# Kernel optimization log

Measured on AMD Instinct MI355X. Metric: run time of the kernel, lower is better.

## Reference

```python
import jax, jax.numpy as jnp
import numpy as np

B, P, K, HE, HF = 256, 128, 512, 1024, 512
D = K + HE + 2 * HF  # 2560, MLP input dim
HID = 64


def setup_inputs() -> dict:
    key = jax.random.key(0)
    ks = jax.random.split(key, 6)
    query = jax.random.normal(ks[0], (B, 1, HE), dtype=jnp.float32)
    keys = jax.random.normal(ks[1], (B, P, K), dtype=jnp.float32)
    frameLSTM_h = jax.random.normal(ks[2], (B, 1, 2 * HF), dtype=jnp.float32)
    mask = jax.random.randint(ks[3], (B, P), 0, 2, dtype=jnp.int32)
    mask = mask.at[:, 0].set(1)  # guarantee at least one unmasked player per row
    W1 = jax.random.normal(ks[4], (D, HID), dtype=jnp.float32) / np.float32(np.sqrt(D))
    W2 = jax.random.normal(ks[5], (HID, 1), dtype=jnp.float32) / np.float32(np.sqrt(HID))
    return dict(query=query, keys=keys, frameLSTM_h=frameLSTM_h, mask=mask, W1=W1, W2=W2)


def reference(query, keys, frameLSTM_h, mask, W1, W2):
    # Faithful to: cat([keys, query.repeat, frame.repeat]) @ W1 -> ReLU -> @ W2.
    # The pre-activation is linear, so splitting W1 by row-blocks is exactly the
    # same math without materializing the repeated/concatenated (B,P,D) tensor.
    W1k = W1[:K]            # (K, 64)
    W1q = W1[K:K + HE]      # (HE, 64)
    W1f = W1[K + HE:]       # (2*HF, 64)
    h = jax.nn.relu(
        jnp.einsum('bpk,kh->bph', keys, W1k)
        + jnp.einsum('boe,eh->boh', query, W1q)        # broadcasts over P
        + jnp.einsum('bof,fh->boh', frameLSTM_h, W1f)  # broadcasts over P
    )  # (B, P, 64)
    raw_scores = jnp.einsum('bph,ho->bp', h, W2)  # (B, P)
    raw_scores = jnp.where(mask == 0, -jnp.inf, raw_scores)
    weights = jax.nn.softmax(raw_scores, axis=1)  # (B, P)
    context = jnp.einsum('bp,bpk->bk', weights, keys)[:, None, :]  # (B, 1, K)
    embeddings = jnp.concatenate([context, frameLSTM_h], axis=2)   # (B, 1, K+2*HF)
    return embeddings, weights
```

## Files before the change

kernel.cpp:

```cpp
#include <hip/hip_runtime.h>
#include <hip/hip_bf16.h>
#include <cstdint>
#include <math.h>


typedef __bf16 bf16;
typedef __attribute__((ext_vector_type(8))) __bf16 bf16x8;
typedef __attribute__((ext_vector_type(4))) float f32x4;

#define NB 256
#define NP 128
#define NK 512
#define SMEM_BYTES (65536 + 8192 + 8192 + 512 + 512 + 65536)

__global__ __launch_bounds__(512, 2) void fused_kernel(
    const float* __restrict__ keys, const float* __restrict__ query,
    const float* __restrict__ frame, const int* __restrict__ mask,
    const float* __restrict__ W1, const float* __restrict__ W2,
    float* __restrict__ out)
{
    extern __shared__ char smem[];
    char* sB      = smem;
    float* sq     = (float*)(smem + 65536);
    float* aux    = sq + 2048;
    float* scores = aux + 2048;
    float* wts    = scores + 128;
    char* kb      = smem + 65536 + 8192 + 8192 + 1024;

    const int b = blockIdx.x;
    const int t = threadIdx.x;
    const int w = t >> 6;
    const int lane = t & 63;
    const int m = lane & 15;
    const int q = lane >> 4;
    const int p0 = w * 16;
    const int xorv = (m & 7) << 4;

    {
        const int d = t * 4;
        const float* src = (d < 1024) ? (query + (size_t)b * 1024 + d)
                                      : (frame + (size_t)b * 1024 + (d - 1024));
        *(float4*)&sq[d] = *(const float4*)src;
    }

    {
#pragma unroll
        for (int i = 0; i < 8; i++) {
            const int id = t + 512 * i;
            const int h = id & 63;
            const int kc = id >> 6;
            float v[8];
#pragma unroll
            for (int j = 0; j < 8; j++)
                v[j] = W1[(size_t)(kc * 8 + j) * 64 + h];
            bf16x8 bv;
#pragma unroll
            for (int j = 0; j < 8; j++) bv[j] = (bf16)v[j];
            *(bf16x8*)(sB + ((h * 1024 + kc * 16) ^ ((h & 7) << 4))) = bv;
        }
    }

    const float* kbase = keys + (size_t)b * (NP * NK);
    float4 kvs[4];
#pragma unroll
    for (int s = 0; s < 4; s++) {
        const int rl = s * 4 + (lane >> 4);
        const int cc = (lane & 15) ^ (rl & 7);
        kvs[s] = *(const float4*)(kbase + (size_t)(p0 + rl) * NK + cc * 4);
    }
    __syncthreads();

    {
        const int s = t >> 4;
        const int j = t & 15;
        const float4* w1f4 = (const float4*)W1;
        float4 pa = {0.f, 0.f, 0.f, 0.f};
#pragma unroll
        for (int bt = 0; bt < 8; bt++) {
            float4 vv[8];
#pragma unroll
            for (int i = 0; i < 8; i++)
                vv[i] = w1f4[(size_t)(512 + s * 64 + bt * 8 + i) * 16 + j];
#pragma unroll
            for (int i = 0; i < 8; i++) {
                const float qv = sq[s * 64 + bt * 8 + i];
                pa.x += qv * vv[i].x; pa.y += qv * vv[i].y;
                pa.z += qv * vv[i].z; pa.w += qv * vv[i].w;
            }
        }
        pa.x += __shfl_xor(pa.x, 16); pa.y += __shfl_xor(pa.y, 16);
        pa.z += __shfl_xor(pa.z, 16); pa.w += __shfl_xor(pa.w, 16);
        pa.x += __shfl_xor(pa.x, 32); pa.y += __shfl_xor(pa.y, 32);
        pa.z += __shfl_xor(pa.z, 32); pa.w += __shfl_xor(pa.w, 32);
        if (lane < 16)
            *(float4*)&aux[w * 64 + lane * 4] = pa;
    }
    __syncthreads();

    float pv[4], wv[4];
#pragma unroll
    for (int nt = 0; nt < 4; nt++) {
        const int h = nt * 16 + m;
        float sacc = 0.f;
#pragma unroll
        for (int ww = 0; ww < 8; ww++) sacc += aux[ww * 64 + h];
        pv[nt] = sacc;
        wv[nt] = W2[h];
    }

    char* kbw = kb + w * 8192;
#pragma unroll
    for (int s = 0; s < 4; s++)
        *(float4*)(kbw + s * 1024 + lane * 16) = kvs[s];

    f32x4 acc[4];
#pragma unroll
    for (int nt = 0; nt < 4; nt++) acc[nt] = (f32x4){0.f, 0.f, 0.f, 0.f};

    bf16x8 Bp[2][4];
#pragma unroll
    for (int nt = 0; nt < 4; nt++)
        Bp[0][nt] = *(const bf16x8*)(sB + nt * 16384 + m * 1024 + ((q * 16) ^ xorv));

#pragma unroll
    for (int c = 0; c < 8; c++) {
        if (c < 7) {
#pragma unroll
            for (int s = 0; s < 4; s++) {
                const int rl = s * 4 + (lane >> 4);
                const int cc = (lane & 15) ^ (rl & 7);
                kvs[s] = *(const float4*)(kbase + (size_t)(p0 + rl) * NK
                                          + (c + 1) * 64 + cc * 4);
            }
        }
        const char* kbr = kbw + (c & 1) * 4096;
#pragma unroll
        for (int kk2 = 0; kk2 < 2; kk2++) {
            const int kkg = c * 2 + kk2;
            const int bc = kkg & 1;
            const int a0 = (m * 256 + kk2 * 128 + q * 32) ^ xorv;
            const float4 f0 = *(const float4*)(kbr + a0);
            const float4 f1 = *(const float4*)(kbr + (a0 ^ 16));
            if (kkg < 15) {
#pragma unroll
                for (int nt = 0; nt < 4; nt++)
                    Bp[bc ^ 1][nt] = *(const bf16x8*)(sB + nt * 16384 + m * 1024
                                      + ((((kkg + 1) * 64) | (q * 16)) ^ xorv));
            }
            bf16x8 Af;
            Af[0] = (bf16)f0.x; Af[1] = (bf16)f0.y;
            Af[2] = (bf16)f0.z; Af[3] = (bf16)f0.w;
            Af[4] = (bf16)f1.x; Af[5] = (bf16)f1.y;
            Af[6] = (bf16)f1.z; Af[7] = (bf16)f1.w;
#pragma unroll
            for (int nt = 0; nt < 4; nt++)
                acc[nt] = __builtin_amdgcn_mfma_f32_16x16x32_bf16(Af, Bp[bc][nt], acc[nt], 0, 0, 0);
        }
        if (c < 7) {
            char* kbwn = kbw + ((c + 1) & 1) * 4096;
#pragma unroll
            for (int s = 0; s < 4; s++)
                *(float4*)(kbwn + s * 1024 + lane * 16) = kvs[s];
        }
    }

    float pr[4] = {0.f, 0.f, 0.f, 0.f};
#pragma unroll
    for (int nt = 0; nt < 4; nt++)
#pragma unroll
        for (int r = 0; r < 4; r++)
            pr[r] += fmaxf(acc[nt][r] + pv[nt], 0.f) * wv[nt];

#pragma unroll
    for (int off = 1; off < 16; off <<= 1)
#pragma unroll
        for (int r = 0; r < 4; r++)
            pr[r] += __shfl_xor(pr[r], off);

    if (m == 0) {
#pragma unroll
        for (int r = 0; r < 4; r++) scores[p0 + q * 4 + r] = pr[r];
    }
    __syncthreads();

    const int cq = t & 127;
    const int pg = t >> 7;
    const float4* kp4 = (const float4*)kbase;
    float4 kv0[8];
#pragma unroll
    for (int i = 0; i < 8; i++)
        kv0[i] = kp4[(size_t)(pg * 32 + i) * 128 + cq];

    if (t < 64) {
        const int pa_ = t, pb_ = t + 64;
        float s0 = (mask[b * 128 + pa_] == 0) ? -INFINITY : scores[pa_];
        float s1 = (mask[b * 128 + pb_] == 0) ? -INFINITY : scores[pb_];
        float mx = fmaxf(s0, s1);
#pragma unroll
        for (int off = 32; off; off >>= 1) mx = fmaxf(mx, __shfl_xor(mx, off));
        float e0 = __expf(s0 - mx), e1 = __expf(s1 - mx);
        float sum = e0 + e1;
#pragma unroll
        for (int off = 32; off; off >>= 1) sum += __shfl_xor(sum, off);
        const float inv = 1.0f / sum;
        e0 *= inv; e1 *= inv;
        wts[pa_] = e0; wts[pb_] = e1;
        float* wout = out + (size_t)NB * 1536;
        wout[b * 128 + pa_] = e0;
        wout[b * 128 + pb_] = e1;
    }
    __syncthreads();

    {
        float4 ca = {0.f, 0.f, 0.f, 0.f};
#pragma unroll
        for (int i = 0; i < 8; i++) {
            const float wvv = wts[pg * 32 + i];
            ca.x += wvv * kv0[i].x; ca.y += wvv * kv0[i].y;
            ca.z += wvv * kv0[i].z; ca.w += wvv * kv0[i].w;
        }
#pragma unroll
        for (int bt = 1; bt < 4; bt++) {
            float4 kv[8];
#pragma unroll
            for (int i = 0; i < 8; i++)
                kv[i] = kp4[(size_t)(pg * 32 + bt * 8 + i) * 128 + cq];
#pragma unroll
            for (int i = 0; i < 8; i++) {
                const float wvv = wts[pg * 32 + bt * 8 + i];
                ca.x += wvv * kv[i].x; ca.y += wvv * kv[i].y;
                ca.z += wvv * kv[i].z; ca.w += wvv * kv[i].w;
            }
        }
        *(float4*)&aux[pg * 512 + cq * 4] = ca;
    }
    __syncthreads();
    if (t < 512)
        out[(size_t)b * 1536 + t] =
            aux[t] + aux[512 + t] + aux[1024 + t] + aux[1536 + t];

    if (t < 256) {
        const float4 fv = *(const float4*)(frame + (size_t)b * 1024 + t * 4);
        *(float4*)(out + (size_t)b * 1536 + 512 + t * 4) = fv;
    }
}

extern "C" void kernel_launch(void* const* d_in, const int* in_sizes, int n_in,
                              void* d_out, int out_size, void* d_ws, size_t ws_size,
                              hipStream_t stream) {
    const float* query = (const float*)d_in[0];
    const float* keys  = (const float*)d_in[1];
    const float* frame = (const float*)d_in[2];
    const int*   mask  = (const int*)d_in[3];
    const float* W1    = (const float*)d_in[4];
    const float* W2    = (const float*)d_in[5];
    float* out = (float*)d_out;

    hipFuncSetAttribute((const void*)fused_kernel,
                        hipFuncAttributeMaxDynamicSharedMemorySize, SMEM_BYTES);

    fused_kernel<<<256, 512, SMEM_BYTES, stream>>>(keys, query, frame, mask,
                                                   W1, W2, out);
}
```

Measured before the change: 123.4 us.

## Stage keys via direct global-to-LDS loads and overlap query projection with MFMA loop

Keys chunks now go straight from global memory into double-buffered LDS through global_load_lds, instead of being loaded into registers and then written to LDS. The query/frame projection against W1, which used to run as a separate phase behind an extra barrier, is now spread across the eight MFMA chunk iterations so its global W1 reads overlap the matrix work. The register double-buffering of the W1 B fragments is dropped, and those fragments are read from LDS right before each MFMA. This lowers register pressure and removes a barrier, at the risk of exposing LDS read latency and depending on correct wait handling for the asynchronous LDS loads.

```diff
diff --git a/kernel.cpp b/kernel.cpp
--- a/kernel.cpp
+++ b/kernel.cpp
@@ -11,7 +11,21 @@
 #define NB 256
 #define NP 128
 #define NK 512
-#define SMEM_BYTES (65536 + 8192 + 8192 + 512 + 512 + 65536)
+#define SMEM_BYTES (65536 + 65536 + 8192 + 8192 + 512 + 512)
+
+#define STAGE_CHUNK(C, PAR)                                                   \
+    {                                                                         \
+        _Pragma("unroll")                                                     \
+        for (int i_ = 0; i_ < 4; i_++) {                                      \
+            const int r4_ = p0 + i_ * 4 + (lane >> 4);                        \
+            const int sc_ = (lane & 15) ^ (r4_ & 7);                          \
+            const float* g_ = kbase + (size_t)r4_ * NK + (C) * 64 + sc_ * 4;  \
+            char* l_ = kb + (PAR) * 32768 + w * 4096 + i_ * 1024;             \
+            __builtin_amdgcn_global_load_lds(                                 \
+                (const __attribute__((address_space(1))) uint32_t*)g_,        \
+                (__attribute__((address_space(3))) uint32_t*)l_, 16, 0, 0);   \
+        }                                                                     \
+    }
 
 __global__ __launch_bounds__(512, 2) void fused_kernel(
     const float* __restrict__ keys, const float* __restrict__ query,
@@ -21,11 +35,11 @@
 {
     extern __shared__ char smem[];
     char* sB      = smem;
-    float* sq     = (float*)(smem + 65536);
+    char* kb      = smem + 65536;
+    float* sq     = (float*)(smem + 131072);
     float* aux    = sq + 2048;
     float* scores = aux + 2048;
     float* wts    = scores + 128;
-    char* kb      = smem + 65536 + 8192 + 8192 + 1024;
 
     const int b = blockIdx.x;
     const int t = threadIdx.x;
@@ -35,6 +49,7 @@
     const int q = lane >> 4;
     const int p0 = w * 16;
     const int xorv = (m & 7) << 4;
+    const float* kbase = keys + (size_t)b * (NP * NK);
 
     {
         const int d = t * 4;
@@ -60,117 +75,75 @@
         }
     }
 
-    const float* kbase = keys + (size_t)b * (NP * NK);
-    float4 kvs[4];
-#pragma unroll
-    for (int s = 0; s < 4; s++) {
-        const int rl = s * 4 + (lane >> 4);
-        const int cc = (lane & 15) ^ (rl & 7);
-        kvs[s] = *(const float4*)(kbase + (size_t)(p0 + rl) * NK + cc * 4);
-    }
-    __syncthreads();
-
-    {
-        const int s = t >> 4;
-        const int j = t & 15;
-        const float4* w1f4 = (const float4*)W1;
-        float4 pa = {0.f, 0.f, 0.f, 0.f};
-#pragma unroll
-        for (int bt = 0; bt < 8; bt++) {
-            float4 vv[8];
-#pragma unroll
-            for (int i = 0; i < 8; i++)
-                vv[i] = w1f4[(size_t)(512 + s * 64 + bt * 8 + i) * 16 + j];
-#pragma unroll
-            for (int i = 0; i < 8; i++) {
-                const float qv = sq[s * 64 + bt * 8 + i];
-                pa.x += qv * vv[i].x; pa.y += qv * vv[i].y;
-                pa.z += qv * vv[i].z; pa.w += qv * vv[i].w;
-            }
-        }
-        pa.x += __shfl_xor(pa.x, 16); pa.y += __shfl_xor(pa.y, 16);
-        pa.z += __shfl_xor(pa.z, 16); pa.w += __shfl_xor(pa.w, 16);
-        pa.x += __shfl_xor(pa.x, 32); pa.y += __shfl_xor(pa.y, 32);
-        pa.z += __shfl_xor(pa.z, 32); pa.w += __shfl_xor(pa.w, 32);
-        if (lane < 16)
-            *(float4*)&aux[w * 64 + lane * 4] = pa;
-    }
-    __syncthreads();
-
-    float pv[4], wv[4];
-#pragma unroll
-    for (int nt = 0; nt < 4; nt++) {
-        const int h = nt * 16 + m;
-        float sacc = 0.f;
-#pragma unroll
-        for (int ww = 0; ww < 8; ww++) sacc += aux[ww * 64 + h];
-        pv[nt] = sacc;
-        wv[nt] = W2[h];
-    }
-
-    char* kbw = kb + w * 8192;
-#pragma unroll
-    for (int s = 0; s < 4; s++)
-        *(float4*)(kbw + s * 1024 + lane * 16) = kvs[s];
+    STAGE_CHUNK(0, 0);
+    __syncthreads();
+
+    const int s5 = t >> 4;
+    const int jq = t & 15;
+    const float4* w1f4 = (const float4*)W1;
+    float4 pa4 = {0.f, 0.f, 0.f, 0.f};
 
     f32x4 acc[4];
 #pragma unroll
     for (int nt = 0; nt < 4; nt++) acc[nt] = (f32x4){0.f, 0.f, 0.f, 0.f};
 
-    bf16x8 Bp[2][4];
-#pragma unroll
-    for (int nt = 0; nt < 4; nt++)
-        Bp[0][nt] = *(const bf16x8*)(sB + nt * 16384 + m * 1024 + ((q * 16) ^ xorv));
-
 #pragma unroll
     for (int c = 0; c < 8; c++) {
-        if (c < 7) {
-#pragma unroll
-            for (int s = 0; s < 4; s++) {
-                const int rl = s * 4 + (lane >> 4);
-                const int cc = (lane & 15) ^ (rl & 7);
-                kvs[s] = *(const float4*)(kbase + (size_t)(p0 + rl) * NK
-                                          + (c + 1) * 64 + cc * 4);
-            }
-        }
-        const char* kbr = kbw + (c & 1) * 4096;
+        const char* kbr = kb + (c & 1) * 32768 + w * 4096;
 #pragma unroll
         for (int kk2 = 0; kk2 < 2; kk2++) {
             const int kkg = c * 2 + kk2;
-            const int bc = kkg & 1;
-            const int a0 = (m * 256 + kk2 * 128 + q * 32) ^ xorv;
+            const int a0 = m * 256 + ((kk2 * 128 + q * 32) ^ xorv);
             const float4 f0 = *(const float4*)(kbr + a0);
             const float4 f1 = *(const float4*)(kbr + (a0 ^ 16));
-            if (kkg < 15) {
-#pragma unroll
-                for (int nt = 0; nt < 4; nt++)
-                    Bp[bc ^ 1][nt] = *(const bf16x8*)(sB + nt * 16384 + m * 1024
-                                      + ((((kkg + 1) * 64) | (q * 16)) ^ xorv));
-            }
             bf16x8 Af;
             Af[0] = (bf16)f0.x; Af[1] = (bf16)f0.y;
             Af[2] = (bf16)f0.z; Af[3] = (bf16)f0.w;
             Af[4] = (bf16)f1.x; Af[5] = (bf16)f1.y;
             Af[6] = (bf16)f1.z; Af[7] = (bf16)f1.w;
 #pragma unroll
-            for (int nt = 0; nt < 4; nt++)
-                acc[nt] = __builtin_amdgcn_mfma_f32_16x16x32_bf16(Af, Bp[bc][nt], acc[nt], 0, 0, 0);
-        }
-        if (c < 7) {
-            char* kbwn = kbw + ((c + 1) & 1) * 4096;
-#pragma unroll
-            for (int s = 0; s < 4; s++)
-                *(float4*)(kbwn + s * 1024 + lane * 16) = kvs[s];
-        }
-    }
+            for (int nt = 0; nt < 4; nt++) {
+                const bf16x8 Bf = *(const bf16x8*)(sB + nt * 16384 + m * 1024
+                                   + (((kkg * 64) | (q * 16)) ^ xorv));
+                acc[nt] = __builtin_amdgcn_mfma_f32_16x16x32_bf16(Af, Bf, acc[nt], 0, 0, 0);
+            }
+        }
+        if (c < 7) STAGE_CHUNK(c + 1, (c + 1) & 1);
+        {
+            const int d0 = c * 256 + s5 * 8;
+            float4 vv[8];
+#pragma unroll
+            for (int i = 0; i < 8; i++)
+                vv[i] = w1f4[(size_t)(512 + d0 + i) * 16 + jq];
+#pragma unroll
+            for (int i = 0; i < 8; i++) {
+                const float qv = sq[d0 + i];
+                pa4.x += qv * vv[i].x; pa4.y += qv * vv[i].y;
+                pa4.z += qv * vv[i].z; pa4.w += qv * vv[i].w;
+            }
+        }
+    }
+
+    pa4.x += __shfl_xor(pa4.x, 16); pa4.y += __shfl_xor(pa4.y, 16);
+    pa4.z += __shfl_xor(pa4.z, 16); pa4.w += __shfl_xor(pa4.w, 16);
+    pa4.x += __shfl_xor(pa4.x, 32); pa4.y += __shfl_xor(pa4.y, 32);
+    pa4.z += __shfl_xor(pa4.z, 32); pa4.w += __shfl_xor(pa4.w, 32);
+    if (lane < 16)
+        *(float4*)&aux[w * 64 + lane * 4] = pa4;
+    __syncthreads();
 
     float pr[4] = {0.f, 0.f, 0.f, 0.f};
 #pragma unroll
-    for (int nt = 0; nt < 4; nt++)
+    for (int nt = 0; nt < 4; nt++) {
+        const int h = nt * 16 + m;
+        float pvh = 0.f;
+#pragma unroll
+        for (int ww = 0; ww < 8; ww++) pvh += aux[ww * 64 + h];
+        const float wvh = W2[h];
 #pragma unroll
         for (int r = 0; r < 4; r++)
-            pr[r] += fmaxf(acc[nt][r] + pv[nt], 0.f) * wv[nt];
-
+            pr[r] += fmaxf(acc[nt][r] + pvh, 0.f) * wvh;
+    }
 #pragma unroll
     for (int off = 1; off < 16; off <<= 1)
 #pragma unroll
```

After: 120.4 us. 1.02x faster.
